# Kernel tuning notes

Measured on AMD Instinct MI355X. Metric: run time of the kernel, lower is better.

The kernel has to match this reference:

```python
import jax, jax.numpy as jnp
import numpy as np

TEMP = 1.0
EPS = 1e-8
DIM = 1024
CODEBOOK_SIZE = 8192
N = 8192


def setup_inputs() -> dict:
    key = jax.random.key(0)
    k_h, k_cb, k_w, k_b = jax.random.split(key, 4)
    h = jax.random.normal(k_h, (N, DIM), dtype=jnp.float32)
    codebook = jax.random.normal(k_cb, (CODEBOOK_SIZE, DIM), dtype=jnp.float32)
    # RMSNorm scale initialized to ones (as in the torch module)
    scale = jnp.ones((DIM,), dtype=jnp.float32)
    # nn.Linear(dim, dim): weight [out, in], bias [out]
    bound = 1.0 / np.sqrt(DIM)
    W = jax.random.uniform(k_w, (DIM, DIM), dtype=jnp.float32, minval=-bound, maxval=bound)
    b = jax.random.uniform(k_b, (DIM,), dtype=jnp.float32, minval=-bound, maxval=bound)
    return {"h": h, "codebook": codebook, "scale": scale, "W": W, "b": b}


def reference(h, codebook, scale, W, b):
    # Squared distances via GEMM identity: ||h-c||^2 = ||h||^2 + ||c||^2 - 2 h.c
    h_sq = jnp.sum(h * h, axis=-1, keepdims=True)              # [N, 1]
    c_sq = jnp.sum(codebook * codebook, axis=-1)               # [K]
    dist = h_sq + c_sq[None, :] - 2.0 * (h @ codebook.T)       # [N, K]
    q = jax.nn.softmax(-dist / TEMP, axis=-1)                  # [N, K]
    z_e = q @ codebook                                         # [N, D]
    # residual MLP: RMSNorm then Linear
    r = h - z_e
    rms = jnp.sqrt(jnp.mean(r * r, axis=-1, keepdims=True))
    x = r / (rms + EPS) * scale
    z_q = z_e + x @ W.T + b
    return z_q
```

## Files before the change

kernel.cpp:

```cpp
#include <hip/hip_runtime.h>

typedef unsigned short u16;
typedef signed char s8;
typedef __attribute__((ext_vector_type(8))) short bf16x8;
typedef __attribute__((ext_vector_type(4))) float f32x4;
typedef __attribute__((ext_vector_type(4))) int i32x4;

__device__ __forceinline__ u16 f2bf(float x) {
  unsigned int u = __float_as_uint(x);
  u = u + 0x7FFFu + ((u >> 16) & 1u);
  return (u16)(u >> 16);
}
__device__ __forceinline__ float bf2f(u16 v) {
  return __uint_as_float(((unsigned int)v) << 16);
}

typedef const __attribute__((address_space(1))) void gas_void;
typedef __attribute__((address_space(3))) void las_void;

__device__ __forceinline__ void gld_lds16(const void* g, void* l) {
  __builtin_amdgcn_global_load_lds((gas_void*)g, (las_void*)l, 16, 0, 0);
}

#define BM 128
#define BN 128
#define BK 64
#define CAP 512
#define DELTA 56.0f

__global__ __launch_bounds__(256) void gemm_c8(
    const s8* __restrict__ A0, const s8* __restrict__ B0,
    u16* __restrict__ S, const float* __restrict__ c_sq) {
  __shared__ __align__(16) s8 lA[128 * 128];
  __shared__ __align__(16) s8 lB[128 * 128];
  int tid = threadIdx.x, wave = tid >> 6, lane = tid & 63;
  long bm = (long)blockIdx.y * 128, bn = (long)blockIdx.x * 128;
  int wm = (wave >> 1) * 64, wn = (wave & 1) * 64;
  int r15 = lane & 15, kg = lane >> 4;
  int srow = wave * 8 + (lane >> 3);
  int scol = ((lane & 7) ^ (lane >> 3)) * 16;

  i32x4 acc[4][4];
#pragma unroll
  for (int i = 0; i < 4; ++i)
#pragma unroll
    for (int j = 0; j < 4; ++j) acc[i][j] = (i32x4){0, 0, 0, 0};

  const s8* ap = A0 + bm * 1024;
  const s8* bp = B0 + bn * 1024;

  for (int k0 = 0; k0 < 1024; k0 += 128) {
    __syncthreads();
#pragma unroll
    for (int c = 0; c < 4; ++c) {
      long go = (long)(c * 32 + srow) * 1024 + k0 + scol;
      int ldoff = c * 4096 + wave * 1024;
      gld_lds16(ap + go, lA + ldoff);
      gld_lds16(bp + go, lB + ldoff);
    }
    __syncthreads();
#pragma unroll
    for (int kk = 0; kk < 2; ++kk) {
      int cb = ((kk * 4 + kg) ^ (r15 & 7)) * 16;
      i32x4 bf[4];
#pragma unroll
      for (int j = 0; j < 4; ++j)
        bf[j] = *(const i32x4*)&lB[(wn + j * 16 + r15) * 128 + cb];
#pragma unroll
      for (int i = 0; i < 4; ++i) {
        i32x4 af = *(const i32x4*)&lA[(wm + i * 16 + r15) * 128 + cb];
#pragma unroll
        for (int j = 0; j < 4; ++j)
          acc[i][j] = __builtin_amdgcn_mfma_i32_16x16x64_i8(af, bf[j], acc[i][j], 0, 0, 0);
      }
    }
  }

#pragma unroll
  for (int i = 0; i < 4; ++i) {
    long rg = bm + wm + i * 16 + kg * 4;
#pragma unroll
    for (int j = 0; j < 4; ++j) {
      long cg = bn + wn + j * 16 + r15;
      float csq = c_sq[cg];
      i32x4 m = acc[i][j];
#pragma unroll
      for (int r = 0; r < 4; ++r)
        S[(rg + r) * 8192 + cg] = f2bf(csq - (float)m[r] * 0.0078125f - 1024.f);
    }
  }
}

__device__ __forceinline__ void stage_tile(const u16* __restrict__ src, long lda,
                                           long row0, long k0, u16* ldst,
                                           int wave, int lane) {
  int srow = wave * 8 + (lane >> 3);
  int scol = ((lane & 7) ^ (lane >> 3)) * 8;
#pragma unroll
  for (int c = 0; c < 4; ++c) {
    const u16* g = src + (row0 + c * 32 + srow) * lda + k0 + scol;
    gld_lds16(g, ldst + c * 2048 + wave * 512);
  }
}

__global__ __launch_bounds__(256) void gemm_zq(
    const u16* __restrict__ A0, long lda,
    const u16* __restrict__ B0, long ldb,
    float* __restrict__ C, long ldc, int K,
    const float* __restrict__ aux0, const float* __restrict__ aux1) {
  __shared__ __align__(16) u16 lA0[BM * BK];
  __shared__ __align__(16) u16 lB0[BN * BK];

  int tid = threadIdx.x;
  int wave = tid >> 6, lane = tid & 63;
  long bm = (long)blockIdx.y * BM, bn = (long)blockIdx.x * BN;
  int wm = (wave >> 1) * 64, wn = (wave & 1) * 64;
  int r15 = lane & 15, kg = lane >> 4;

  f32x4 acc[4][4];
#pragma unroll
  for (int i = 0; i < 4; ++i)
#pragma unroll
    for (int j = 0; j < 4; ++j) acc[i][j] = (f32x4){0.f, 0.f, 0.f, 0.f};

  for (int k0 = 0; k0 < K; k0 += BK) {
    __syncthreads();
    stage_tile(A0, lda, bm, k0, lA0, wave, lane);
    stage_tile(B0, ldb, bn, k0, lB0, wave, lane);
    __syncthreads();

#pragma unroll
    for (int kk = 0; kk < 2; ++kk) {
      int cu = ((kk * 4 + kg) ^ (r15 & 7)) * 8;
      bf16x8 ah[4], bh[4];
#pragma unroll
      for (int i = 0; i < 4; ++i) {
        ah[i] = *(const bf16x8*)&lA0[(wm + i * 16 + r15) * 64 + cu];
        bh[i] = *(const bf16x8*)&lB0[(wn + i * 16 + r15) * 64 + cu];
      }
#pragma unroll
      for (int i = 0; i < 4; ++i)
#pragma unroll
        for (int j = 0; j < 4; ++j)
          acc[i][j] = __builtin_amdgcn_mfma_f32_16x16x32_bf16(ah[i], bh[j], acc[i][j], 0, 0, 0);
    }
  }

#pragma unroll
  for (int i = 0; i < 4; ++i) {
    long rg = bm + wm + i * 16 + kg * 4;
#pragma unroll
    for (int j = 0; j < 4; ++j) {
      long cg = bn + wn + j * 16 + r15;
      f32x4 v = acc[i][j];
      float bb = aux1[cg];
#pragma unroll
      for (int r = 0; r < 4; ++r)
        C[(rg + r) * ldc + cg] = v[r] + aux0[(rg + r) * ldc + cg] + bb;
    }
  }
}

__device__ __forceinline__ int q8(float x) {
  float q = rintf(x * 16.f);
  q = fminf(fmaxf(q, -127.f), 127.f);
  return (int)q;
}

__global__ __launch_bounds__(256) void prep_h_i8(const float* __restrict__ in,
                                                 s8* __restrict__ q0, int n4) {
  int i = blockIdx.x * 256 + threadIdx.x;
  if (i >= n4) return;
  float4 v = ((const float4*)in)[i];
  unsigned int w = (unsigned int)((q8(v.x) & 0xFF) | ((q8(v.y) & 0xFF) << 8) |
                                  ((q8(v.z) & 0xFF) << 16) | ((q8(v.w) & 0xFF) << 24));
  ((unsigned int*)q0)[i] = w;
}

__global__ __launch_bounds__(256) void prep_cb_i8(const float* __restrict__ cb,
                                                  s8* __restrict__ q0,
                                                  float* __restrict__ c_sq) {
  long k = blockIdx.x;
  int t = threadIdx.x, lane = t & 63, wave = t >> 6;
  float4 v = ((const float4*)(cb + k * 1024))[t];
  unsigned int w = (unsigned int)((q8(v.x) & 0xFF) | ((q8(v.y) & 0xFF) << 8) |
                                  ((q8(v.z) & 0xFF) << 16) | ((q8(v.w) & 0xFF) << 24));
  ((unsigned int*)(q0 + k * 1024))[t] = w;
  float ss = v.x * v.x + v.y * v.y + v.z * v.z + v.w * v.w;
#pragma unroll
  for (int o = 32; o; o >>= 1) ss += __shfl_xor(ss, o);
  __shared__ float sc[4];
  if (lane == 0) sc[wave] = ss;
  __syncthreads();
  if (t == 0) c_sq[k] = sc[0] + sc[1] + sc[2] + sc[3];
}

__global__ __launch_bounds__(256) void prep_bf16(const float* __restrict__ in,
                                                 u16* __restrict__ o, int n4) {
  int i = blockIdx.x * 256 + threadIdx.x;
  if (i >= n4) return;
  float4 v = ((const float4*)in)[i];
  ushort4 h;
  h.x = f2bf(v.x); h.y = f2bf(v.y); h.z = f2bf(v.z); h.w = f2bf(v.w);
  ((ushort4*)o)[i] = h;
}

__global__ __launch_bounds__(256) void scan_rows(const u16* __restrict__ S,
                                                 int* __restrict__ cand,
                                                 int* __restrict__ cnt) {
  long m = blockIdx.x;
  int t = threadIdx.x, lane = t & 63, wave = t >> 6;
  const u16* row = S + m * 8192;
  ushort4 v[8];
#pragma unroll
  for (int i = 0; i < 8; ++i) v[i] = ((const ushort4*)row)[i * 256 + t];
  float mn = 3.0e38f;
#pragma unroll
  for (int i = 0; i < 8; ++i)
    mn = fminf(mn, fminf(fminf(bf2f(v[i].x), bf2f(v[i].y)),
                         fminf(bf2f(v[i].z), bf2f(v[i].w))));
#pragma unroll
  for (int o = 32; o; o >>= 1) mn = fminf(mn, __shfl_xor(mn, o));
  __shared__ float sm[4];
  __shared__ int wsum[4];
  if (lane == 0) sm[wave] = mn;
  __syncthreads();
  mn = fminf(fminf(sm[0], sm[1]), fminf(sm[2], sm[3]));
  float thr = mn + DELTA;
  int c = 0;
#pragma unroll
  for (int i = 0; i < 8; ++i)
    c += (bf2f(v[i].x) <= thr) + (bf2f(v[i].y) <= thr) +
         (bf2f(v[i].z) <= thr) + (bf2f(v[i].w) <= thr);
  int pre = c;
#pragma unroll
  for (int o = 1; o < 64; o <<= 1) {
    int y = __shfl_up(pre, o);
    if (lane >= o) pre += y;
  }
  if (lane == 63) wsum[wave] = pre;
  __syncthreads();
  int base = 0;
#pragma unroll
  for (int w = 0; w < 4; ++w) base += (w < wave) ? wsum[w] : 0;
  int pos = base + pre - c;
#pragma unroll
  for (int i = 0; i < 8; ++i) {
    u16 q[4] = {v[i].x, v[i].y, v[i].z, v[i].w};
#pragma unroll
    for (int j = 0; j < 4; ++j) {
      if (bf2f(q[j]) <= thr) {
        if (pos < CAP) cand[m * CAP + pos] = i * 1024 + t * 4 + j;
        ++pos;
      }
    }
  }
  if (t == 0) {
    int tot = wsum[0] + wsum[1] + wsum[2] + wsum[3];
    cnt[m] = tot < CAP ? tot : CAP;
  }
}

__global__ __launch_bounds__(256) void refine_rms(
    const float* __restrict__ h, const float* __restrict__ cb,
    const float* __restrict__ csq, const int* __restrict__ cand,
    const int* __restrict__ cnt, const float* __restrict__ scale,
    float* __restrict__ z_e, u16* __restrict__ x) {
  long m = blockIdx.x;
  int t = threadIdx.x, lane = t & 63, wave = t >> 6;
  int n = cnt[m];
  __shared__ float sm[4], ssum[4], sc[4];
  __shared__ float lacc[4][1024];
  const float4* h4 = (const float4*)(h + m * 1024);
  float4 hw[4];
#pragma unroll
  for (int i = 0; i < 4; ++i) hw[i] = h4[lane * 4 + i];

  float mw = -3.0e38f, sw = 0.f;
  float4 a0 = {0.f, 0.f, 0.f, 0.f}, a1 = a0, a2 = a0, a3 = a0;
  for (int j = wave; j < n; j += 4) {
    long k = cand[m * CAP + j];
    const float4* c4 = (const float4*)(cb + k * 1024);
    float4 cv0 = c4[lane * 4 + 0], cv1 = c4[lane * 4 + 1];
    float4 cv2 = c4[lane * 4 + 2], cv3 = c4[lane * 4 + 3];
    float d = hw[0].x * cv0.x + hw[0].y * cv0.y + hw[0].z * cv0.z + hw[0].w * cv0.w +
              hw[1].x * cv1.x + hw[1].y * cv1.y + hw[1].z * cv1.z + hw[1].w * cv1.w +
              hw[2].x * cv2.x + hw[2].y * cv2.y + hw[2].z * cv2.z + hw[2].w * cv2.w +
              hw[3].x * cv3.x + hw[3].y * cv3.y + hw[3].z * cv3.z + hw[3].w * cv3.w;
#pragma unroll
    for (int o = 32; o; o >>= 1) d += __shfl_xor(d, o);
    float lg = 2.f * d - csq[k];
    if (lg > mw) {
      float r = __expf(mw - lg);
      sw *= r;
      a0.x *= r; a0.y *= r; a0.z *= r; a0.w *= r;
      a1.x *= r; a1.y *= r; a1.z *= r; a1.w *= r;
      a2.x *= r; a2.y *= r; a2.z *= r; a2.w *= r;
      a3.x *= r; a3.y *= r; a3.z *= r; a3.w *= r;
      mw = lg;
    }
    float w = __expf(lg - mw);
    sw += w;
    a0.x += w * cv0.x; a0.y += w * cv0.y; a0.z += w * cv0.z; a0.w += w * cv0.w;
    a1.x += w * cv1.x; a1.y += w * cv1.y; a1.z += w * cv1.z; a1.w += w * cv1.w;
    a2.x += w * cv2.x; a2.y += w * cv2.y; a2.z += w * cv2.z; a2.w += w * cv2.w;
    a3.x += w * cv3.x; a3.y += w * cv3.y; a3.z += w * cv3.z; a3.w += w * cv3.w;
  }
  if (lane == 0) { sm[wave] = mw; ssum[wave] = sw; }
  __syncthreads();
  float M = fmaxf(fmaxf(sm[0], sm[1]), fmaxf(sm[2], sm[3]));
  float Stot = ssum[0] * __expf(sm[0] - M) + ssum[1] * __expf(sm[1] - M) +
               ssum[2] * __expf(sm[2] - M) + ssum[3] * __expf(sm[3] - M);
  float rw = __expf(mw - M);
  float* lw = &lacc[wave][lane * 16];
  *(float4*)(lw + 0) = (float4){a0.x * rw, a0.y * rw, a0.z * rw, a0.w * rw};
  *(float4*)(lw + 4) = (float4){a1.x * rw, a1.y * rw, a1.z * rw, a1.w * rw};
  *(float4*)(lw + 8) = (float4){a2.x * rw, a2.y * rw, a2.z * rw, a2.w * rw};
  *(float4*)(lw + 12) = (float4){a3.x * rw, a3.y * rw, a3.z * rw, a3.w * rw};
  __syncthreads();
  float rs = 1.f / Stot;
  float4 p0 = *(const float4*)&lacc[0][t * 4];
  float4 p1 = *(const float4*)&lacc[1][t * 4];
  float4 p2 = *(const float4*)&lacc[2][t * 4];
  float4 p3 = *(const float4*)&lacc[3][t * 4];
  float4 ze;
  ze.x = (p0.x + p1.x + p2.x + p3.x) * rs;
  ze.y = (p0.y + p1.y + p2.y + p3.y) * rs;
  ze.z = (p0.z + p1.z + p2.z + p3.z) * rs;
  ze.w = (p0.w + p1.w + p2.w + p3.w) * rs;
  *(float4*)(z_e + m * 1024 + t * 4) = ze;
  float4 hv = h4[t];
  float4 r;
  r.x = hv.x - ze.x; r.y = hv.y - ze.y; r.z = hv.z - ze.z; r.w = hv.w - ze.w;
  float ss = r.x * r.x + r.y * r.y + r.z * r.z + r.w * r.w;
#pragma unroll
  for (int o = 32; o; o >>= 1) ss += __shfl_xor(ss, o);
  if (lane == 0) sc[wave] = ss;
  __syncthreads();
  float tot = sc[0] + sc[1] + sc[2] + sc[3];
  float inv = 1.f / (sqrtf(tot * (1.f / 1024.f)) + 1e-8f);
  float4 s4 = ((const float4*)scale)[t];
  ushort4 o;
  o.x = f2bf(r.x * inv * s4.x); o.y = f2bf(r.y * inv * s4.y);
  o.z = f2bf(r.z * inv * s4.z); o.w = f2bf(r.w * inv * s4.w);
  *(ushort4*)(x + m * 1024 + t * 4) = o;
}

extern "C" void kernel_launch(void* const* d_in, const int* in_sizes, int n_in,
                              void* d_out, int out_size, void* d_ws, size_t ws_size,
                              hipStream_t stream) {
  const float* h = (const float*)d_in[0];
  const float* cb = (const float*)d_in[1];
  const float* scale = (const float*)d_in[2];
  const float* W = (const float*)d_in[3];
  const float* b = (const float*)d_in[4];
  float* out = (float*)d_out;

  char* ws = (char*)d_ws;
  size_t off = 0;
  auto alloc = [&](size_t bytes) -> char* {
    char* p = ws + off;
    off = (off + bytes + 255) & ~(size_t)255;
    return p;
  };
  s8* h8 = (s8*)alloc(8192L * 1024);
  s8* c8 = (s8*)alloc(8192L * 1024);
  u16* Wbf = (u16*)alloc(1024L * 1024 * 2);
  float* c_sq = (float*)alloc(8192L * 4);
  float* z_e = (float*)alloc(8192L * 1024 * 4);
  u16* x = (u16*)alloc(8192L * 1024 * 2);
  int* cand = (int*)alloc(8192L * CAP * 4);
  int* cnt = (int*)alloc(8192L * 4);
  u16* Sbf = (u16*)alloc(8192L * 8192 * 2);

  prep_h_i8<<<8192, 256, 0, stream>>>(h, h8, 2097152);
  prep_cb_i8<<<8192, 256, 0, stream>>>(cb, c8, c_sq);
  prep_bf16<<<1024, 256, 0, stream>>>(W, Wbf, 262144);

  gemm_c8<<<dim3(64, 64), 256, 0, stream>>>(h8, c8, Sbf, c_sq);
  scan_rows<<<8192, 256, 0, stream>>>(Sbf, cand, cnt);
  refine_rms<<<8192, 256, 0, stream>>>(h, cb, c_sq, cand, cnt, scale, z_e, x);
  gemm_zq<<<dim3(8, 64), 256, 0, stream>>>(x, 1024L, Wbf, 1024L,
                                           out, 1024L, 1024, z_e, b);
}
```

Before: 227.4 us.

## Quantize score matrix to uint8 and double-buffer LDS in int8 GEMM

Result: slower. 258.1 us (+13.5%).

```diff
diff --git a/kernel.cpp b/kernel.cpp
--- a/kernel.cpp
+++ b/kernel.cpp
@@ -1,6 +1,7 @@
 #include <hip/hip_runtime.h>
 
 typedef unsigned short u16;
+typedef unsigned char u8;
 typedef signed char s8;
 typedef __attribute__((ext_vector_type(8))) short bf16x8;
 typedef __attribute__((ext_vector_type(4))) float f32x4;
@@ -26,13 +27,13 @@
 #define BN 128
 #define BK 64
 #define CAP 512
-#define DELTA 56.0f
+#define DU8 14
 
 __global__ __launch_bounds__(256) void gemm_c8(
     const s8* __restrict__ A0, const s8* __restrict__ B0,
-    u16* __restrict__ S, const float* __restrict__ c_sq) {
-  __shared__ __align__(16) s8 lA[128 * 128];
-  __shared__ __align__(16) s8 lB[128 * 128];
+    u8* __restrict__ S, const float* __restrict__ c_sq) {
+  __shared__ __align__(16) s8 lA[2][128 * 128];
+  __shared__ __align__(16) s8 lB[2][128 * 128];
   int tid = threadIdx.x, wave = tid >> 6, lane = tid & 63;
   long bm = (long)blockIdx.y * 128, bn = (long)blockIdx.x * 128;
   int wm = (wave >> 1) * 64, wn = (wave & 1) * 64;
@@ -40,40 +41,49 @@
   int srow = wave * 8 + (lane >> 3);
   int scol = ((lane & 7) ^ (lane >> 3)) * 16;
 
-  i32x4 acc[4][4];
-#pragma unroll
-  for (int i = 0; i < 4; ++i)
-#pragma unroll
-    for (int j = 0; j < 4; ++j) acc[i][j] = (i32x4){0, 0, 0, 0};
-
   const s8* ap = A0 + bm * 1024;
   const s8* bp = B0 + bn * 1024;
 
-  for (int k0 = 0; k0 < 1024; k0 += 128) {
-    __syncthreads();
+  i32x4 acc[4][4];
+#pragma unroll
+  for (int i = 0; i < 4; ++i)
+#pragma unroll
+    for (int j = 0; j < 4; ++j) acc[i][j] = (i32x4){0, 0, 0, 0};
+
+  auto STAGE = [&](int buf, int k0) {
 #pragma unroll
     for (int c = 0; c < 4; ++c) {
       long go = (long)(c * 32 + srow) * 1024 + k0 + scol;
       int ldoff = c * 4096 + wave * 1024;
-      gld_lds16(ap + go, lA + ldoff);
-      gld_lds16(bp + go, lB + ldoff);
-    }
-    __syncthreads();
+      gld_lds16(ap + go, lA[buf] + ldoff);
+      gld_lds16(bp + go, lB[buf] + ldoff);
+    }
+  };
+
+  STAGE(0, 0);
+  __syncthreads();
+  int cur = 0;
+  for (int k0 = 0; k0 < 1024; k0 += 128) {
+    if (k0 < 896) STAGE(cur ^ 1, k0 + 128);
+    const s8* la = lA[cur];
+    const s8* lb = lB[cur];
 #pragma unroll
     for (int kk = 0; kk < 2; ++kk) {
       int cb = ((kk * 4 + kg) ^ (r15 & 7)) * 16;
       i32x4 bf[4];
 #pragma unroll
       for (int j = 0; j < 4; ++j)
-        bf[j] = *(const i32x4*)&lB[(wn + j * 16 + r15) * 128 + cb];
+        bf[j] = *(const i32x4*)&lb[(wn + j * 16 + r15) * 128 + cb];
 #pragma unroll
       for (int i = 0; i < 4; ++i) {
-        i32x4 af = *(const i32x4*)&lA[(wm + i * 16 + r15) * 128 + cb];
+        i32x4 af = *(const i32x4*)&la[(wm + i * 16 + r15) * 128 + cb];
 #pragma unroll
         for (int j = 0; j < 4; ++j)
           acc[i][j] = __builtin_amdgcn_mfma_i32_16x16x64_i8(af, bf[j], acc[i][j], 0, 0, 0);
       }
     }
+    __syncthreads();
+    cur ^= 1;
   }
 
 #pragma unroll
@@ -85,8 +95,12 @@
       float csq = c_sq[cg];
       i32x4 m = acc[i][j];
 #pragma unroll
-      for (int r = 0; r < 4; ++r)
-        S[(rg + r) * 8192 + cg] = f2bf(csq - (float)m[r] * 0.0078125f - 1024.f);
+      for (int r = 0; r < 4; ++r) {
+        float v = csq - (float)m[r] * 0.0078125f;
+        int q = (int)rintf((v - 1024.f) * 0.25f) + 128;
+        q = q < 0 ? 0 : (q > 255 ? 255 : q);
+        S[(rg + r) * 8192 + cg] = (u8)q;
+      }
     }
   }
 }
@@ -205,33 +219,39 @@
   ((ushort4*)o)[i] = h;
 }
 
-__global__ __launch_bounds__(256) void scan_rows(const u16* __restrict__ S,
+__global__ __launch_bounds__(256) void scan_rows(const u8* __restrict__ S,
                                                  int* __restrict__ cand,
                                                  int* __restrict__ cnt) {
   long m = blockIdx.x;
   int t = threadIdx.x, lane = t & 63, wave = t >> 6;
-  const u16* row = S + m * 8192;
-  ushort4 v[8];
-#pragma unroll
-  for (int i = 0; i < 8; ++i) v[i] = ((const ushort4*)row)[i * 256 + t];
-  float mn = 3.0e38f;
+  const uint4* row4 = (const uint4*)(S + m * 8192);
+  uint4 va = row4[t], vb = row4[256 + t];
+  unsigned int w[8] = {va.x, va.y, va.z, va.w, vb.x, vb.y, vb.z, vb.w};
+  int bmin = 255;
 #pragma unroll
   for (int i = 0; i < 8; ++i)
-    mn = fminf(mn, fminf(fminf(bf2f(v[i].x), bf2f(v[i].y)),
-                         fminf(bf2f(v[i].z), bf2f(v[i].w))));
-#pragma unroll
-  for (int o = 32; o; o >>= 1) mn = fminf(mn, __shfl_xor(mn, o));
-  __shared__ float sm[4];
+#pragma unroll
+    for (int j = 0; j < 4; ++j) {
+      int b = (w[i] >> (8 * j)) & 0xFF;
+      bmin = b < bmin ? b : bmin;
+    }
+#pragma unroll
+  for (int o = 32; o; o >>= 1) {
+    int y = __shfl_xor(bmin, o);
+    bmin = y < bmin ? y : bmin;
+  }
+  __shared__ int sm[4];
   __shared__ int wsum[4];
-  if (lane == 0) sm[wave] = mn;
-  __syncthreads();
-  mn = fminf(fminf(sm[0], sm[1]), fminf(sm[2], sm[3]));
-  float thr = mn + DELTA;
+  if (lane == 0) sm[wave] = bmin;
+  __syncthreads();
+  bmin = min(min(sm[0], sm[1]), min(sm[2], sm[3]));
+  int thr = bmin + DU8;
   int c = 0;
 #pragma unroll
   for (int i = 0; i < 8; ++i)
-    c += (bf2f(v[i].x) <= thr) + (bf2f(v[i].y) <= thr) +
-         (bf2f(v[i].z) <= thr) + (bf2f(v[i].w) <= thr);
+#pragma unroll
+    for (int j = 0; j < 4; ++j)
+      c += (((w[i] >> (8 * j)) & 0xFF) <= (unsigned)thr);
   int pre = c;
 #pragma unroll
   for (int o = 1; o < 64; o <<= 1) {
@@ -242,19 +262,19 @@
   __syncthreads();
   int base = 0;
 #pragma unroll
-  for (int w = 0; w < 4; ++w) base += (w < wave) ? wsum[w] : 0;
+  for (int wv = 0; wv < 4; ++wv) base += (wv < wave) ? wsum[wv] : 0;
   int pos = base + pre - c;
 #pragma unroll
-  for (int i = 0; i < 8; ++i) {
-    u16 q[4] = {v[i].x, v[i].y, v[i].z, v[i].w};
+  for (int i = 0; i < 8; ++i)
 #pragma unroll
     for (int j = 0; j < 4; ++j) {
-      if (bf2f(q[j]) <= thr) {
-        if (pos < CAP) cand[m * CAP + pos] = i * 1024 + t * 4 + j;
+      int b = (w[i] >> (8 * j)) & 0xFF;
+      if (b <= thr) {
+        int col = (i < 4 ? t * 16 : 4096 + t * 16) + (i & 3) * 4 + j;
+        if (pos < CAP) cand[m * CAP + pos] = col;
         ++pos;
       }
     }
-  }
   if (t == 0) {
     int tot = wsum[0] + wsum[1] + wsum[2] + wsum[3];
     cnt[m] = tot < CAP ? tot : CAP;
@@ -371,14 +391,14 @@
   u16* x = (u16*)alloc(8192L * 1024 * 2);
   int* cand = (int*)alloc(8192L * CAP * 4);
   int* cnt = (int*)alloc(8192L * 4);
-  u16* Sbf = (u16*)alloc(8192L * 8192 * 2);
+  u8* Sq = (u8*)alloc(8192L * 8192);
 
   prep_h_i8<<<8192, 256, 0, stream>>>(h, h8, 2097152);
   prep_cb_i8<<<8192, 256, 0, stream>>>(cb, c8, c_sq);
   prep_bf16<<<1024, 256, 0, stream>>>(W, Wbf, 262144);
 
-  gemm_c8<<<dim3(64, 64), 256, 0, stream>>>(h8, c8, Sbf, c_sq);
-  scan_rows<<<8192, 256, 0, stream>>>(Sbf, cand, cnt);
+  gemm_c8<<<dim3(64, 64), 256, 0, stream>>>(h8, c8, Sq, c_sq);
+  scan_rows<<<8192, 256, 0, stream>>>(Sq, cand, cnt);
   refine_rms<<<8192, 256, 0, stream>>>(h, cb, c_sq, cand, cnt, scale, z_e, x);
   gemm_zq<<<dim3(8, 64), 256, 0, stream>>>(x, 1024L, Wbf, 1024L,
                                            out, 1024L, 1024, z_e, b);
```
